# Kernel tuning notes

Measured on AMD Instinct MI355X. Metric: run time of the kernel, lower is better.

The kernel has to match this reference:

```python
import jax, jax.numpy as jnp
import numpy as np

DIM = 1024
NUM_HEADS = 16
HEAD_DIM = DIM // NUM_HEADS
FF = 4 * DIM
B, T, S = 8, 512, 4096


def setup_inputs() -> dict:
    key = jax.random.key(0)
    ks = jax.random.split(key, 14)
    sc = 1.0 / np.sqrt(DIM)
    inp = {
        "x": jax.random.normal(ks[0], (B, T, DIM), jnp.float32),
        "inp": jax.random.normal(ks[1], (B, S, DIM), jnp.float32),
        # attention projections
        "Wq": jax.random.normal(ks[2], (DIM, DIM), jnp.float32) * sc,
        "bq": jnp.zeros((DIM,), jnp.float32),
        "Wk": jax.random.normal(ks[3], (DIM, DIM), jnp.float32) * sc,
        "bk": jnp.zeros((DIM,), jnp.float32),
        "Wv": jax.random.normal(ks[4], (DIM, DIM), jnp.float32) * sc,
        "bv": jnp.zeros((DIM,), jnp.float32),
        "Wo": jax.random.normal(ks[5], (DIM, DIM), jnp.float32) * sc,
        "bo": jnp.zeros((DIM,), jnp.float32),
        # MLP
        "W1": jax.random.normal(ks[6], (DIM, FF), jnp.float32) * sc,
        "b1": jnp.zeros((FF,), jnp.float32),
        "W2": jax.random.normal(ks[7], (FF, DIM), jnp.float32) * (1.0 / np.sqrt(FF)),
        "b2": jnp.zeros((DIM,), jnp.float32),
    }
    return inp


def _perceiver_layer(x, inp, Wq, bq, Wk, bk, Wv, bv, Wo, bo, W1, b1, W2, b2):
    b, t, _ = x.shape
    s = inp.shape[1]
    q = (x @ Wq + bq).reshape(b, t, NUM_HEADS, HEAD_DIM)
    k = (inp @ Wk + bk).reshape(b, s, NUM_HEADS, HEAD_DIM)
    v = (inp @ Wv + bv).reshape(b, s, NUM_HEADS, HEAD_DIM)
    # [b, h, t, s] score tensor (as in original code)
    attn = jnp.einsum('bthd,bshd->bhts', q, k)
    attn = jax.nn.softmax(attn / jnp.sqrt(jnp.float32(HEAD_DIM)), axis=-1)
    out = jnp.einsum('bhts,bshd->bthd', attn, v).reshape(b, t, DIM)
    attn_out = out @ Wo + bo
    x = x + attn_out
    h = jax.nn.gelu(x @ W1 + b1, approximate=True)  # flax nn.gelu default is tanh approx
    x = x + (h @ W2 + b2)
    return x


def reference(x, inp, Wq, bq, Wk, bk, Wv, bv, Wo, bo, W1, b1, W2, b2):
    return _perceiver_layer(x, inp, Wq, bq, Wk, bk, Wv, bv, Wo, bo, W1, b1, W2, b2)
```

## Files before the change

### kernel.cpp

```cpp
#include <hip/hip_runtime.h>
#include <hip/hip_bf16.h>

#define DIM 1024
#define NHEADS 16
#define HDIM 64
#define FF_ 4096
#define BB 8
#define TT 512
#define SS 4096

typedef __attribute__((ext_vector_type(8))) __bf16 bf16x8;
typedef __attribute__((ext_vector_type(4))) float f32x4;
typedef __attribute__((ext_vector_type(4))) unsigned short us4;

#define SWZ(r, b) ((b) ^ (((r) & 7) << 4))

typedef const __attribute__((address_space(1))) void gvoid_t;
typedef __attribute__((address_space(3))) void lvoid_t;

__device__ __forceinline__ void ldst16(const void* g, void* l) {
  __builtin_amdgcn_global_load_lds((gvoid_t*)g, (lvoid_t*)l, 16, 0, 0);
}

__device__ inline unsigned short f2bf(float f) {
  unsigned u = __float_as_uint(f);
  u += 0x7fff + ((u >> 16) & 1);
  return (unsigned short)(u >> 16);
}

__device__ __forceinline__ unsigned cvt_pk(float lo, float hi) {
  unsigned r;
  asm("v_cvt_pk_bf16_f32 %0, %1, %2" : "=v"(r) : "v"(lo), "v"(hi));
  return r;
}

__global__ void cvt_f32_bf16(const float* __restrict__ in,
                             unsigned short* __restrict__ out, int n4) {
  int i = blockIdx.x * blockDim.x + threadIdx.x;
  int stride = gridDim.x * blockDim.x;
  for (; i < n4; i += stride) {
    float4 v = ((const float4*)in)[i];
    uint2 w = {cvt_pk(v.x, v.y), cvt_pk(v.z, v.w)};
    ((uint2*)out)[i] = w;
  }
}

__global__ void transpose_f32_bf16(const float* __restrict__ in,
                                   unsigned short* __restrict__ out,
                                   int R, int C) {
  __shared__ float tile[32][33];
  int bc = blockIdx.x * 32, br = blockIdx.y * 32;
  int tx = threadIdx.x & 31, ty = threadIdx.x >> 5;
#pragma unroll
  for (int i = 0; i < 32; i += 8)
    tile[ty + i][tx] = in[(size_t)(br + ty + i) * C + bc + tx];
  __syncthreads();
#pragma unroll
  for (int i = 0; i < 32; i += 8)
    out[(size_t)(bc + ty + i) * R + br + tx] = f2bf(tile[tx][ty + i]);
}

template <int EPI>
__global__ __launch_bounds__(256, 3)
void gemm_kernel(const unsigned short* __restrict__ A,
                 const unsigned short* __restrict__ Bt,
                 const float* __restrict__ bias,
                 const float* __restrict__ res,
                 void* __restrict__ Cp,
                 unsigned short* __restrict__ C2,
                 int M, int N, int K) {
  __shared__ char smem[32768];
  char* As = smem;
  char* Bs = smem + 16384;

  const int tid = threadIdx.x;
  const int lane = tid & 63;
  const int wave = tid >> 6;
  const int wm = wave >> 1, wn = wave & 1;

  const int flat = blockIdx.y * gridDim.x + blockIdx.x;
  const int cpx = (gridDim.x * gridDim.y) >> 3;
  const int swz = (flat & 7) * cpx + (flat >> 3);
  const int m0 = (swz / gridDim.x) * 128, n0 = (swz % gridDim.x) * 128;

  f32x4 acc[4][4];
#pragma unroll
  for (int i = 0; i < 4; ++i)
#pragma unroll
    for (int j = 0; j < 4; ++j) acc[i][j] = (f32x4){0.f, 0.f, 0.f, 0.f};

  for (int k0 = 0; k0 < K; k0 += 64) {
    __syncthreads();
#pragma unroll
    for (int i = 0; i < 4; ++i) {
      int ch = (wave * 4 + i) * 64 + lane;
      int r = ch >> 3, c8 = (ch & 7) ^ (r & 7);
      ldst16(A + (size_t)(m0 + r) * K + k0 + c8 * 8, As + (wave * 4 + i) * 1024);
      ldst16(Bt + (size_t)(n0 + r) * K + k0 + c8 * 8, Bs + (wave * 4 + i) * 1024);
    }
    __syncthreads();

#pragma unroll
    for (int kk = 0; kk < 2; ++kk) {
      bf16x8 a[4], b[4];
#pragma unroll
      for (int mi = 0; mi < 4; ++mi) {
        int r = wm * 64 + mi * 16 + (lane & 15);
        a[mi] = *(const bf16x8*)(As + r * 128 + SWZ(r, kk * 64 + (lane >> 4) * 16));
      }
#pragma unroll
      for (int ni = 0; ni < 4; ++ni) {
        int r = wn * 64 + ni * 16 + (lane & 15);
        b[ni] = *(const bf16x8*)(Bs + r * 128 + SWZ(r, kk * 64 + (lane >> 4) * 16));
      }
#pragma unroll
      for (int mi = 0; mi < 4; ++mi)
#pragma unroll
        for (int ni = 0; ni < 4; ++ni)
          acc[mi][ni] = __builtin_amdgcn_mfma_f32_16x16x32_bf16(b[ni], a[mi], acc[mi][ni], 0, 0, 0);
    }
  }

  const int q = lane & 15, g4 = (lane >> 4) * 4;
#pragma unroll
  for (int mi = 0; mi < 4; ++mi) {
    int row = m0 + wm * 64 + mi * 16 + q;
#pragma unroll
    for (int ni = 0; ni < 4; ++ni) {
      int colb = n0 + wn * 64 + ni * 16 + g4;
      float4 bv = *(const float4*)(bias + colb);
      f32x4 v = acc[mi][ni];
      float v0 = v[0] + bv.x, v1 = v[1] + bv.y, v2 = v[2] + bv.z, v3 = v[3] + bv.w;
      if (EPI == 0) {
        uint2 w = {cvt_pk(v0, v1), cvt_pk(v2, v3)};
        *(uint2*)((unsigned short*)Cp + (size_t)row * N + colb) = w;
      } else if (EPI == 1) {
        float o[4] = {v0, v1, v2, v3};
#pragma unroll
        for (int j = 0; j < 4; ++j) {
          float u = 0.7978845608028654f * (o[j] + 0.044715f * o[j] * o[j] * o[j]);
          float e = __expf(2.f * u);
          float th = 1.f - 2.f / (e + 1.f);
          o[j] = 0.5f * o[j] * (1.f + th);
        }
        uint2 w = {cvt_pk(o[0], o[1]), cvt_pk(o[2], o[3])};
        *(uint2*)((unsigned short*)Cp + (size_t)row * N + colb) = w;
      } else {
        float4 r4 = *(const float4*)(res + (size_t)row * N + colb);
        float o0 = v0 + r4.x, o1 = v1 + r4.y, o2 = v2 + r4.z, o3 = v3 + r4.w;
        float4 ov = {o0, o1, o2, o3};
        *(float4*)((float*)Cp + (size_t)row * N + colb) = ov;
        if (EPI == 3) {
          uint2 w = {cvt_pk(o0, o1), cvt_pk(o2, o3)};
          *(uint2*)(C2 + (size_t)row * N + colb) = w;
        }
      }
    }
  }
}

template <int EPI>
__global__ __launch_bounds__(512, 2)
void gemm256(const unsigned short* __restrict__ A,
             const unsigned short* __restrict__ Bt,
             const float* __restrict__ bias,
             void* __restrict__ Cp,
             unsigned short* __restrict__ C2,
             int M, int N, int K) {
  __shared__ char smem[131072];

  const int tid = threadIdx.x, lane = tid & 63, wave = tid >> 6;
  const int q = lane & 15, g = lane >> 4;
  const int wm = wave >> 2, wn = wave & 3;

  const int flat = blockIdx.y * gridDim.x + blockIdx.x;
  const int cpx = (gridDim.x * gridDim.y) >> 3;
  const int swz = (flat & 7) * cpx + (flat >> 3);
  const int m0 = (swz / gridDim.x) * 256, n0 = (swz % gridDim.x) * 256;

  const unsigned short* Arow = A + (size_t)m0 * K;
  const unsigned short* Brow = Bt + (size_t)n0 * K;

  const int r0 = tid >> 3, c0 = ((tid & 7) ^ (r0 & 7)) * 8;
  const int r1 = (tid + 512) >> 3, c1 = (((tid + 512) & 7) ^ (r1 & 7)) * 8;

#define STA(buf, half, kt)                                                     \
  { char* d = smem + (buf) * 32768 + (half) * 16384;                           \
    const unsigned short* s = Arow + (size_t)((half) * 128) * K + (kt) * 64;   \
    ldst16(s + (size_t)r0 * K + c0, d + tid * 16);                             \
    ldst16(s + (size_t)r1 * K + c1, d + 8192 + tid * 16); }
#define STB(buf, half, kt)                                                     \
  { char* d = smem + 65536 + (buf) * 32768 + (half) * 16384;                   \
    const unsigned short* s = Brow + (size_t)((half) * 128) * K + (kt) * 64;   \
    ldst16(s + (size_t)r0 * K + c0, d + tid * 16);                             \
    ldst16(s + (size_t)r1 * K + c1, d + 8192 + tid * 16); }

  f32x4 acc[8][4];
#pragma unroll
  for (int i = 0; i < 8; ++i)
#pragma unroll
    for (int j = 0; j < 4; ++j) acc[i][j] = (f32x4){0.f, 0.f, 0.f, 0.f};

  STA(0, 0, 0); STA(0, 1, 0); STB(0, 0, 0); STB(0, 1, 0);
  STB(1, 0, 1); STB(1, 1, 1); STA(1, 0, 1);
  asm volatile("s_waitcnt vmcnt(6)" ::: "memory");
  __builtin_amdgcn_s_barrier();

  const int NKT = K >> 6;
  for (int kt = 0; kt < NKT; ++kt) {
    const int cb = kt & 1, nb = cb ^ 1;
    const char* Ab = smem + cb * 32768;
    const char* Bb = smem + 65536 + cb * 32768;
    bf16x8 bfr[4][2];

#pragma unroll
    for (int p = 0; p < 4; ++p) {
      if (p == 0) { if (kt + 1 < NKT) STA(nb, 1, kt + 1); }
      else if (p == 1) { if (kt + 2 < NKT) STB(cb, 0, kt + 2); }
      else if (p == 2) { if (kt + 2 < NKT) STB(cb, 1, kt + 2); }
      else            { if (kt + 2 < NKT) STA(cb, 0, kt + 2); }

      bf16x8 af[2][2];
#pragma unroll
      for (int i = 0; i < 2; ++i)
#pragma unroll
        for (int kk = 0; kk < 2; ++kk) {
          int r = wm * 128 + (2 * p + i) * 16 + q;
          af[i][kk] = *(const bf16x8*)(Ab + r * 128 + SWZ(r, kk * 64 + g * 16));
        }
      if (p == 0) {
#pragma unroll
        for (int nr = 0; nr < 4; ++nr)
#pragma unroll
          for (int kk = 0; kk < 2; ++kk) {
            int r = wn * 64 + nr * 16 + q;
            bfr[nr][kk] = *(const bf16x8*)(Bb + r * 128 + SWZ(r, kk * 64 + g * 16));
          }
      }

      __builtin_amdgcn_s_barrier();
      asm volatile("s_waitcnt lgkmcnt(0)" ::: "memory");
      __builtin_amdgcn_sched_barrier(0);
      __builtin_amdgcn_s_setprio(1);
#pragma unroll
      for (int i = 0; i < 2; ++i)
#pragma unroll
        for (int nr = 0; nr < 4; ++nr)
#pragma unroll
          for (int kk = 0; kk < 2; ++kk)
            acc[2 * p + i][nr] = __builtin_amdgcn_mfma_f32_16x16x32_bf16(
                bfr[nr][kk], af[i][kk], acc[2 * p + i][nr], 0, 0, 0);
      __builtin_amdgcn_s_setprio(0);

      if (p == 1) asm volatile("s_waitcnt vmcnt(10)" ::: "memory");
      if (p == 3) asm volatile("s_waitcnt vmcnt(8)" ::: "memory");
      __builtin_amdgcn_s_barrier();
    }
  }

  const int g4 = g * 4;
#pragma unroll
  for (int mr = 0; mr < 8; ++mr) {
    int row = m0 + wm * 128 + mr * 16 + q;
#pragma unroll
    for (int nr = 0; nr < 4; ++nr) {
      int colb = n0 + wn * 64 + nr * 16 + g4;
      float4 bv = *(const float4*)(bias + colb);
      f32x4 v = acc[mr][nr];
      float v0 = v[0] + bv.x, v1 = v[1] + bv.y, v2 = v[2] + bv.z, v3 = v[3] + bv.w;
      if (EPI == 1) {
        float o[4] = {v0, v1, v2, v3};
#pragma unroll
        for (int j = 0; j < 4; ++j) {
          float u = 0.7978845608028654f * (o[j] + 0.044715f * o[j] * o[j] * o[j]);
          float e = __expf(2.f * u);
          float th = 1.f - 2.f / (e + 1.f);
          o[j] = 0.5f * o[j] * (1.f + th);
        }
        uint2 w = {cvt_pk(o[0], o[1]), cvt_pk(o[2], o[3])};
        *(uint2*)((unsigned short*)Cp + (size_t)row * N + colb) = w;
      } else {
        if (n0 < 1024) {
          uint2 w = {cvt_pk(v0, v1), cvt_pk(v2, v3)};
          *(uint2*)((unsigned short*)Cp + (size_t)row * 1024 + colb) = w;
        } else {
          int b = row >> 12, s = row & 4095;
          int d0 = colb - 1024;
          unsigned short* vt = C2 + ((size_t)b * DIM + d0) * SS + s;
          vt[0] = f2bf(v0);
          vt[SS] = f2bf(v1);
          vt[2 * SS] = f2bf(v2);
          vt[3 * SS] = f2bf(v3);
        }
      }
    }
  }
#undef STA
#undef STB
}

__global__ __launch_bounds__(512, 4)
void attn_kernel3(const unsigned short* __restrict__ Qb,
                  const unsigned short* __restrict__ Kb,
                  const unsigned short* __restrict__ Vt,
                  unsigned short* __restrict__ Ob) {
  __shared__ char smem[65536];

  const int tid = threadIdx.x, lane = tid & 63, wave = tid >> 6;
  const int bid = blockIdx.x;
  const int b = bid & 7, qt = (bid >> 3) & 3, h = bid >> 5;
  const int q0 = qt * 128;
  const int q = lane & 15, g = lane >> 4;

  const int rK = tid >> 3;
  const int cK = (tid & 7) ^ (rK & 7);
  char* const Pw = smem + 49152 + wave * 2048;

  const unsigned short* srcQ = Qb + ((size_t)b * TT + q0) * DIM + h * HDIM;
  const unsigned short* srcK = Kb + (size_t)b * SS * DIM + h * HDIM;
  const unsigned short* srcV = Vt + ((size_t)b * DIM + h * HDIM) * SS;

  {
    int r = tid >> 3, c = (tid & 7) ^ (r & 7);
    ldst16(srcQ + (size_t)r * DIM + c * 8, smem + tid * 16);
    int ch = tid + 512;
    r = ch >> 3; c = (ch & 7) ^ (r & 7);
    ldst16(srcQ + (size_t)r * DIM + c * 8, smem + ch * 16);
  }
  ldst16(srcK + (size_t)rK * DIM + cK * 8, smem + 16384 + tid * 16);
  ldst16(srcV + (size_t)rK * SS + cK * 8, smem + 32768 + tid * 16);
  __syncthreads();

  bf16x8 qf[2];
  {
    int r = wave * 16 + q;
    qf[0] = *(const bf16x8*)(smem + r * 128 + SWZ(r, g * 16));
    qf[1] = *(const bf16x8*)(smem + r * 128 + SWZ(r, 64 + g * 16));
  }

  f32x4 acc[4];
#pragma unroll
  for (int dt = 0; dt < 4; ++dt) acc[dt] = (f32x4){0.f, 0.f, 0.f, 0.f};
  float lsum = 0.f;
  const float CSC = 0.125f * 1.4426950408889634f;

  const int NT = SS / 64;
  for (int t = 0; t < NT; ++t) {
    char* Kc = smem + 16384 + (t & 1) * 8192;
    char* Vc = smem + 32768 + (t & 1) * 8192;
    if (t + 1 < NT) {
      char* Kn = smem + 16384 + ((t + 1) & 1) * 8192;
      char* Vn = smem + 32768 + ((t + 1) & 1) * 8192;
      ldst16(srcK + (size_t)((t + 1) * 64 + rK) * DIM + cK * 8, Kn + tid * 16);
      ldst16(srcV + (size_t)rK * SS + (t + 1) * 64 + cK * 8, Vn + tid * 16);
    }

    f32x4 st[4];
#pragma unroll
    for (int si = 0; si < 4; ++si) st[si] = (f32x4){0.f, 0.f, 0.f, 0.f};
#pragma unroll
    for (int kk = 0; kk < 2; ++kk)
#pragma unroll
      for (int si = 0; si < 4; ++si) {
        int r = si * 16 + q;
        bf16x8 kf = *(const bf16x8*)(Kc + r * 128 + SWZ(r, kk * 64 + g * 16));
        st[si] = __builtin_amdgcn_mfma_f32_16x16x32_bf16(kf, qf[kk], st[si], 0, 0, 0);
      }

    float rs = 0.f;
#pragma unroll
    for (int si = 0; si < 4; ++si) {
      float p0 = __builtin_amdgcn_exp2f(st[si][0] * CSC);
      float p1 = __builtin_amdgcn_exp2f(st[si][1] * CSC);
      float p2 = __builtin_amdgcn_exp2f(st[si][2] * CSC);
      float p3 = __builtin_amdgcn_exp2f(st[si][3] * CSC);
      rs += (p0 + p1) + (p2 + p3);
      uint2 w = {cvt_pk(p0, p1), cvt_pk(p2, p3)};
      *(uint2*)(Pw + q * 128 + SWZ(q, si * 32 + g * 8)) = w;
    }
    lsum += rs;

#pragma unroll
    for (int kk = 0; kk < 2; ++kk) {
      bf16x8 pb = *(const bf16x8*)(Pw + q * 128 + SWZ(q, kk * 64 + g * 16));
#pragma unroll
      for (int dt = 0; dt < 4; ++dt) {
        int r = dt * 16 + q;
        bf16x8 va = *(const bf16x8*)(Vc + r * 128 + SWZ(r, kk * 64 + g * 16));
        acc[dt] = __builtin_amdgcn_mfma_f32_16x16x32_bf16(va, pb, acc[dt], 0, 0, 0);
      }
    }
    __syncthreads();
  }

  lsum += __shfl_xor(lsum, 16);
  lsum += __shfl_xor(lsum, 32);
  float inv = 1.0f / lsum;
#pragma unroll
  for (int dt = 0; dt < 4; ++dt) {
    f32x4 v = acc[dt];
    uint2 w = {cvt_pk(v[0] * inv, v[1] * inv), cvt_pk(v[2] * inv, v[3] * inv)};
    *(uint2*)(Pw + q * 128 + SWZ(q, dt * 32 + g * 8)) = w;
  }
  __builtin_amdgcn_s_waitcnt(0);
  int qr = lane >> 2, cb = (lane & 3) * 32;
  uint4 lo = *(const uint4*)(Pw + qr * 128 + SWZ(qr, cb));
  uint4 hi = *(const uint4*)(Pw + qr * 128 + SWZ(qr, cb + 16));
  size_t ob = ((size_t)b * TT + q0 + wave * 16 + qr) * DIM + h * HDIM + (lane & 3) * 16;
  *(uint4*)(Ob + ob) = lo;
  *(uint4*)(Ob + ob + 8) = hi;
}

extern "C" void kernel_launch(void* const* d_in, const int* in_sizes, int n_in,
                              void* d_out, int out_size, void* d_ws, size_t ws_size,
                              hipStream_t stream) {
  const float* x   = (const float*)d_in[0];
  const float* inp = (const float*)d_in[1];
  const float* Wq  = (const float*)d_in[2];
  const float* bq  = (const float*)d_in[3];
  const float* Wk  = (const float*)d_in[4];
  const float* bk  = (const float*)d_in[5];
  const float* Wv  = (const float*)d_in[6];
  const float* bv  = (const float*)d_in[7];
  const float* Wo  = (const float*)d_in[8];
  const float* bo  = (const float*)d_in[9];
  const float* W1  = (const float*)d_in[10];
  const float* b1  = (const float*)d_in[11];
  const float* W2  = (const float*)d_in[12];
  const float* b2  = (const float*)d_in[13];
  float* out = (float*)d_out;

  char* ws = (char*)d_ws;
  const size_t MB = 1024ull * 1024ull;
  unsigned short* Wqt  = (unsigned short*)(ws + 0 * MB);
  unsigned short* Wkt  = (unsigned short*)(ws + 2 * MB);
  unsigned short* Wvt  = (unsigned short*)(ws + 4 * MB);
  unsigned short* Wkvt = Wkt;
  unsigned short* Wot  = (unsigned short*)(ws + 6 * MB);
  unsigned short* W1t  = (unsigned short*)(ws + 8 * MB);
  unsigned short* W2t  = (unsigned short*)(ws + 16 * MB);
  float*          bkv  = (float*)(ws + 24 * MB);
  unsigned short* Qb   = (unsigned short*)(ws + 25 * MB);
  unsigned short* Kb   = (unsigned short*)(ws + 33 * MB);
  float*          x2   = (float*)(ws + 33 * MB);
  unsigned short* x2b  = (unsigned short*)(ws + 49 * MB);
  unsigned short* hb   = (unsigned short*)(ws + 57 * MB);
  unsigned short* Vt   = (unsigned short*)(ws + 97 * MB);
  unsigned short* inpb = (unsigned short*)(ws + 161 * MB);
  unsigned short* xb   = (unsigned short*)(ws + 225 * MB);
  unsigned short* Obf  = (unsigned short*)d_out;

  hipMemcpyAsync(bkv, bk, 1024 * sizeof(float), hipMemcpyDeviceToDevice, stream);
  hipMemcpyAsync(bkv + 1024, bv, 1024 * sizeof(float), hipMemcpyDeviceToDevice, stream);

  cvt_f32_bf16<<<2048, 256, 0, stream>>>(inp, inpb, BB * SS * DIM / 4);
  cvt_f32_bf16<<<1024, 256, 0, stream>>>(x, xb, BB * TT * DIM / 4);

  transpose_f32_bf16<<<dim3(32, 32), 256, 0, stream>>>(Wq, Wqt, 1024, 1024);
  transpose_f32_bf16<<<dim3(32, 32), 256, 0, stream>>>(Wk, Wkt, 1024, 1024);
  transpose_f32_bf16<<<dim3(32, 32), 256, 0, stream>>>(Wv, Wvt, 1024, 1024);
  transpose_f32_bf16<<<dim3(32, 32), 256, 0, stream>>>(Wo, Wot, 1024, 1024);
  transpose_f32_bf16<<<dim3(128, 32), 256, 0, stream>>>(W1, W1t, 1024, 4096);
  transpose_f32_bf16<<<dim3(32, 128), 256, 0, stream>>>(W2, W2t, 4096, 1024);

  gemm_kernel<0><<<dim3(8, 32), 256, 0, stream>>>(xb, Wqt, bq, nullptr, Qb, nullptr, BB * TT, DIM, DIM);
  gemm256<2><<<dim3(8, 128), 512, 0, stream>>>(inpb, Wkvt, bkv, Kb, Vt, BB * SS, 2048, DIM);

  attn_kernel3<<<dim3(512), 512, 0, stream>>>(Qb, Kb, Vt, Obf);

  gemm_kernel<3><<<dim3(8, 32), 256, 0, stream>>>(Obf, Wot, bo, x, x2, x2b, BB * TT, DIM, DIM);
  gemm256<1><<<dim3(16, 16), 512, 0, stream>>>(x2b, W1t, b1, hb, nullptr, BB * TT, FF_, DIM);
  gemm_kernel<2><<<dim3(8, 32), 256, 0, stream>>>(hb, W2t, b2, x2, out, nullptr, BB * TT, DIM, FF_);
}
```

Measured before the change: 472.0 us.

## Triple-buffer K/V tiles in attention and reschedule gemm256 prefetch waits

The attention kernel moves from double to triple buffering of K/V tiles, prefetching two tiles ahead and replacing the per-iteration __syncthreads with a counted vmcnt wait plus barrier, so global loads overlap more of the compute. Shared memory grows from 64KB to 80KB per block, which may cut occupancy. The gemm256 kernel also changes its prefetch schedule: both A halves of the next tile are issued at p==0, the A-prefetch for kt+2 is dropped, and the waits collapse into one vmcnt wait per k-step, giving less lookahead on A in exchange for fewer waits.

```diff
diff --git a/kernel.cpp b/kernel.cpp
--- a/kernel.cpp
+++ b/kernel.cpp
@@ -202,8 +202,8 @@
     for (int j = 0; j < 4; ++j) acc[i][j] = (f32x4){0.f, 0.f, 0.f, 0.f};
 
   STA(0, 0, 0); STA(0, 1, 0); STB(0, 0, 0); STB(0, 1, 0);
-  STB(1, 0, 1); STB(1, 1, 1); STA(1, 0, 1);
-  asm volatile("s_waitcnt vmcnt(6)" ::: "memory");
+  STB(1, 0, 1); STB(1, 1, 1);
+  asm volatile("s_waitcnt vmcnt(4)" ::: "memory");
   __builtin_amdgcn_s_barrier();
 
   const int NKT = K >> 6;
@@ -215,11 +215,6 @@
 
 #pragma unroll
     for (int p = 0; p < 4; ++p) {
-      if (p == 0) { if (kt + 1 < NKT) STA(nb, 1, kt + 1); }
-      else if (p == 1) { if (kt + 2 < NKT) STB(cb, 0, kt + 2); }
-      else if (p == 2) { if (kt + 2 < NKT) STB(cb, 1, kt + 2); }
-      else            { if (kt + 2 < NKT) STA(cb, 0, kt + 2); }
-
       bf16x8 af[2][2];
 #pragma unroll
       for (int i = 0; i < 2; ++i)
@@ -238,6 +233,10 @@
           }
       }
 
+      if (p == 0)      { if (kt + 1 < NKT) { STA(nb, 0, kt + 1); STA(nb, 1, kt + 1); } }
+      else if (p == 1) { if (kt + 2 < NKT) STB(cb, 0, kt + 2); }
+      else if (p == 2) { if (kt + 2 < NKT) STB(cb, 1, kt + 2); }
+
       __builtin_amdgcn_s_barrier();
       asm volatile("s_waitcnt lgkmcnt(0)" ::: "memory");
       __builtin_amdgcn_sched_barrier(0);
@@ -252,8 +251,10 @@
                 bfr[nr][kk], af[i][kk], acc[2 * p + i][nr], 0, 0, 0);
       __builtin_amdgcn_s_setprio(0);
 
-      if (p == 1) asm volatile("s_waitcnt vmcnt(10)" ::: "memory");
-      if (p == 3) asm volatile("s_waitcnt vmcnt(8)" ::: "memory");
+      if (p == 3) {
+        if (kt + 2 < NKT) { asm volatile("s_waitcnt vmcnt(4)" ::: "memory"); }
+        else              { asm volatile("s_waitcnt vmcnt(0)" ::: "memory"); }
+      }
       __builtin_amdgcn_s_barrier();
     }
   }
@@ -300,11 +301,11 @@
 }
 
 __global__ __launch_bounds__(512, 4)
-void attn_kernel3(const unsigned short* __restrict__ Qb,
+void attn_kernel4(const unsigned short* __restrict__ Qb,
                   const unsigned short* __restrict__ Kb,
                   const unsigned short* __restrict__ Vt,
                   unsigned short* __restrict__ Ob) {
-  __shared__ char smem[65536];
+  __shared__ char smem[81920];
 
   const int tid = threadIdx.x, lane = tid & 63, wave = tid >> 6;
   const int bid = blockIdx.x;
@@ -314,7 +315,7 @@
 
   const int rK = tid >> 3;
   const int cK = (tid & 7) ^ (rK & 7);
-  char* const Pw = smem + 49152 + wave * 2048;
+  char* const Pw = smem + 65536 + wave * 2048;
 
   const unsigned short* srcQ = Qb + ((size_t)b * TT + q0) * DIM + h * HDIM;
   const unsigned short* srcK = Kb + (size_t)b * SS * DIM + h * HDIM;
@@ -328,8 +329,11 @@
     ldst16(srcQ + (size_t)r * DIM + c * 8, smem + ch * 16);
   }
   ldst16(srcK + (size_t)rK * DIM + cK * 8, smem + 16384 + tid * 16);
-  ldst16(srcV + (size_t)rK * SS + cK * 8, smem + 32768 + tid * 16);
-  __syncthreads();
+  ldst16(srcV + (size_t)rK * SS + cK * 8, smem + 40960 + tid * 16);
+  ldst16(srcK + (size_t)(64 + rK) * DIM + cK * 8, smem + 24576 + tid * 16);
+  ldst16(srcV + (size_t)rK * SS + 64 + cK * 8, smem + 49152 + tid * 16);
+  asm volatile("s_waitcnt vmcnt(2)" ::: "memory");
+  __builtin_amdgcn_s_barrier();
 
   bf16x8 qf[2];
   {
@@ -345,14 +349,15 @@
   const float CSC = 0.125f * 1.4426950408889634f;
 
   const int NT = SS / 64;
+  int cur = 0, sb = 2;
   for (int t = 0; t < NT; ++t) {
-    char* Kc = smem + 16384 + (t & 1) * 8192;
-    char* Vc = smem + 32768 + (t & 1) * 8192;
-    if (t + 1 < NT) {
-      char* Kn = smem + 16384 + ((t + 1) & 1) * 8192;
-      char* Vn = smem + 32768 + ((t + 1) & 1) * 8192;
-      ldst16(srcK + (size_t)((t + 1) * 64 + rK) * DIM + cK * 8, Kn + tid * 16);
-      ldst16(srcV + (size_t)rK * SS + (t + 1) * 64 + cK * 8, Vn + tid * 16);
+    char* Kc = smem + 16384 + cur * 8192;
+    char* Vc = smem + 40960 + cur * 8192;
+    if (t + 2 < NT) {
+      char* Kn = smem + 16384 + sb * 8192;
+      char* Vn = smem + 40960 + sb * 8192;
+      ldst16(srcK + (size_t)((t + 2) * 64 + rK) * DIM + cK * 8, Kn + tid * 16);
+      ldst16(srcV + (size_t)rK * SS + (t + 2) * 64 + cK * 8, Vn + tid * 16);
     }
 
     f32x4 st[4];
@@ -390,7 +395,12 @@
         acc[dt] = __builtin_amdgcn_mfma_f32_16x16x32_bf16(va, pb, acc[dt], 0, 0, 0);
       }
     }
-    __syncthreads();
+
+    if (t + 2 < NT) { asm volatile("s_waitcnt vmcnt(2)" ::: "memory"); }
+    else            { asm volatile("s_waitcnt vmcnt(0)" ::: "memory"); }
+    __builtin_amdgcn_s_barrier();
+    cur = cur == 2 ? 0 : cur + 1;
+    sb  = sb  == 2 ? 0 : sb  + 1;
   }
 
   lsum += __shfl_xor(lsum, 16);
@@ -466,7 +476,7 @@
   gemm_kernel<0><<<dim3(8, 32), 256, 0, stream>>>(xb, Wqt, bq, nullptr, Qb, nullptr, BB * TT, DIM, DIM);
   gemm256<2><<<dim3(8, 128), 512, 0, stream>>>(inpb, Wkvt, bkv, Kb, Vt, BB * SS, 2048, DIM);
 
-  attn_kernel3<<<dim3(512), 512, 0, stream>>>(Qb, Kb, Vt, Obf);
+  attn_kernel4<<<dim3(512), 512, 0, stream>>>(Qb, Kb, Vt, Obf);
 
   gemm_kernel<3><<<dim3(8, 32), 256, 0, stream>>>(Obf, Wot, bo, x, x2, x2b, BB * TT, DIM, DIM);
   gemm256<1><<<dim3(16, 16), 512, 0, stream>>>(x2b, W1t, b1, hb, nullptr, BB * TT, FF_, DIM);
```

New measurement: 495.3 us. +4.9%, slower.
